# Performance work log

Hardware: AMD Instinct MI355X
Metric: run time of the kernel (lower is better)

The kernel has to match this reference:

```python
import jax, jax.numpy as jnp
import numpy as np

N = 10000   # nodes
E = 160000  # edges (before self-loops)
IN = 77     # input feature dim
H = 4       # heads (layers 1,2)
C = 128     # per-head out channels


def setup_inputs() -> dict:
    key = jax.random.key(0)
    ks = jax.random.split(key, 16)
    p = lambda k, shape: (jax.random.normal(k, shape, jnp.float32) * 0.1)
    z = lambda n: jnp.zeros((n,), jnp.float32)
    return {
        "x": jax.random.normal(ks[0], (N, IN), jnp.float32),
        "edge_index": jax.random.randint(ks[1], (2, E), 0, N),
        # layer 1: 77 -> H*C
        "Wl1": p(ks[2], (H * C, IN)), "bl1": z(H * C),
        "Wr1": p(ks[3], (H * C, IN)), "br1": z(H * C),
        "att1": p(ks[4], (H, C)), "b1": z(H * C),
        # layer 2: H*C -> H*C
        "Wl2": p(ks[5], (H * C, H * C)), "bl2": z(H * C),
        "Wr2": p(ks[6], (H * C, H * C)), "br2": z(H * C),
        "att2": p(ks[7], (H, C)), "b2": z(H * C),
        # layer 3: H*C -> C (1 head)
        "Wl3": p(ks[8], (C, H * C)), "bl3": z(C),
        "Wr3": p(ks[9], (C, H * C)), "br3": z(C),
        "att3": p(ks[10], (1, C)), "b3": z(C),
    }


def _gatv2_layer(x, src, dst, Wl, bl, Wr, br, att, bias, heads, outc):
    """PyG GATv2Conv (eval mode, self-loops already in src/dst, concat=True)."""
    n = x.shape[0]
    xl = (x @ Wl.T + bl).reshape(n, heads, outc)  # source transform
    xr = (x @ Wr.T + br).reshape(n, heads, outc)  # target transform
    # edge-wise score: a^T LeakyReLU(xl[src] + xr[dst])
    e = jax.nn.leaky_relu(xl[src] + xr[dst], negative_slope=0.2)  # [E,H,C]
    logits = jnp.einsum('ehc,hc->eh', e, att)                      # [E,H]
    # segment softmax over edges grouped by destination node
    m = jax.lax.stop_gradient(jax.ops.segment_max(logits, dst, num_segments=n))
    ev = jnp.exp(logits - m[dst])
    denom = jax.ops.segment_sum(ev, dst, num_segments=n)
    alpha = ev / (denom[dst] + 1e-16)                              # [E,H]
    # scatter-add weighted messages
    out = jax.ops.segment_sum(xl[src] * alpha[:, :, None], dst, num_segments=n)
    return out.reshape(n, heads * outc) + bias


def reference(x, edge_index, Wl1, bl1, Wr1, br1, att1, b1,
              Wl2, bl2, Wr2, br2, att2, b2,
              Wl3, bl3, Wr3, br3, att3, b3):
    n = x.shape[0]
    loop = jnp.arange(n)
    src = jnp.concatenate([edge_index[0], loop])  # add self-loops (PyG default)
    dst = jnp.concatenate([edge_index[1], loop])
    h = jax.nn.elu(_gatv2_layer(x, src, dst, Wl1, bl1, Wr1, br1, att1, b1, H, C))
    h = jax.nn.elu(_gatv2_layer(h, src, dst, Wl2, bl2, Wr2, br2, att2, b2, H, C))
    return _gatv2_layer(h, src, dst, Wl3, bl3, Wr3, br3, att3, b3, 1, C)
```

## Files before the change

### kernel.cpp

```cpp
#include <hip/hip_runtime.h>
#include <hip/hip_bf16.h>
#include <math.h>

typedef __attribute__((ext_vector_type(8))) short short8;
typedef __attribute__((ext_vector_type(4))) float f32x4;
typedef __attribute__((ext_vector_type(2))) float f32x2;
typedef __attribute__((ext_vector_type(4))) unsigned int u32x4;

__device__ __forceinline__ float bf2f(unsigned short u) {
  union { unsigned int i; float f; } x; x.i = ((unsigned int)u) << 16; return x.f;
}

__device__ __forceinline__ f32x2 pk_add(f32x2 a, f32x2 b) {
  f32x2 d; asm("v_pk_add_f32 %0, %1, %2" : "=v"(d) : "v"(a), "v"(b)); return d;
}
__device__ __forceinline__ f32x2 pk_mul(f32x2 a, f32x2 b) {
  f32x2 d; asm("v_pk_mul_f32 %0, %1, %2" : "=v"(d) : "v"(a), "v"(b)); return d;
}
__device__ __forceinline__ f32x2 pk_fma(f32x2 a, f32x2 b, f32x2 c) {
  f32x2 d; asm("v_pk_fma_f32 %0, %1, %2, %3" : "=v"(d) : "v"(a), "v"(b), "v"(c)); return d;
}
__device__ __forceinline__ f32x2 pk_abs(f32x2 a) {
  union { f32x2 f; unsigned int u[2]; } x; x.f = a;
  x.u[0] &= 0x7fffffffu; x.u[1] &= 0x7fffffffu;
  return x.f;
}
__device__ __forceinline__ f32x2 unpk(unsigned int w) {
  union { f32x2 f; unsigned int u[2]; } x;
  x.u[0] = w << 16;
  x.u[1] = w & 0xffff0000u;
  return x.f;
}

template <int CTRL>
__device__ __forceinline__ float dpp_add(float x) {
  int y = __builtin_amdgcn_update_dpp(0, __builtin_bit_cast(int, x), CTRL, 0xF, 0xF, true);
  return x + __builtin_bit_cast(float, y);
}
__device__ __forceinline__ float row16_sum(float p) {
  p = dpp_add<0xB1>(p);
  p = dpp_add<0x4E>(p);
  p = dpp_add<0x124>(p);
  p = dpp_add<0x128>(p);
  return p;
}

__device__ __forceinline__ void load_lds16(const void* g, void* l) {
  __builtin_amdgcn_global_load_lds(
      (const __attribute__((address_space(1))) unsigned int*)g,
      (__attribute__((address_space(3))) unsigned int*)l, 16, 0, 0);
}

__global__ __launch_bounds__(256) void gemm_mfma(
    const __hip_bfloat16* __restrict__ A, const __hip_bfloat16* __restrict__ B,
    const float* __restrict__ bl, const float* __restrict__ br, int halfN,
    __hip_bfloat16* __restrict__ out, int M, int K, int Nout) {
  __shared__ __hip_bfloat16 As[128 * 32];
  __shared__ __hip_bfloat16 Bs[128 * 32];
  int t = threadIdx.x;
  int w = t >> 6, l = t & 63;
  int lr = l & 15, lh = l >> 4;
  int wr = w >> 1, wc = w & 1;
  int m0 = blockIdx.y * 128, n0 = blockIdx.x * 128;
  f32x4 acc[4][4] = {};
  int nk = K >> 5;
  for (int ks = 0; ks < nk; ++ks) {
    int k0 = ks << 5;
#pragma unroll
    for (int p = 0; p < 2; ++p) {
      int c = p * 256 + t;
      int row = c >> 2, sub = c & 3;
      int gm = m0 + row; if (gm >= M) gm = M - 1;
      const __hip_bfloat16* gsrc = A + (size_t)gm * K + k0 + sub * 8;
      char* ldst = (char*)As + (size_t)(p * 256 + w * 64) * 16;
      load_lds16(gsrc, ldst);
    }
#pragma unroll
    for (int p = 0; p < 2; ++p) {
      int c = p * 256 + t;
      int row = c >> 2, sub = c & 3;
      const __hip_bfloat16* gsrc = B + (size_t)(n0 + row) * K + k0 + sub * 8;
      char* ldst = (char*)Bs + (size_t)(p * 256 + w * 64) * 16;
      load_lds16(gsrc, ldst);
    }
    __syncthreads();
    short8 af[4], bf[4];
#pragma unroll
    for (int mt = 0; mt < 4; ++mt)
      af[mt] = *(const short8*)(As + (size_t)(wr * 64 + mt * 16 + lr) * 32 + lh * 8);
#pragma unroll
    for (int nt = 0; nt < 4; ++nt)
      bf[nt] = *(const short8*)(Bs + (size_t)(wc * 64 + nt * 16 + lr) * 32 + lh * 8);
#pragma unroll
    for (int mt = 0; mt < 4; ++mt)
#pragma unroll
      for (int nt = 0; nt < 4; ++nt)
        acc[mt][nt] = __builtin_amdgcn_mfma_f32_16x16x32_bf16(af[mt], bf[nt], acc[mt][nt], 0, 0, 0);
    __syncthreads();
  }
#pragma unroll
  for (int mt = 0; mt < 4; ++mt) {
#pragma unroll
    for (int r = 0; r < 4; ++r) {
      int gm = m0 + wr * 64 + mt * 16 + lh * 4 + r;
      if (gm >= M) continue;
#pragma unroll
      for (int nt = 0; nt < 4; ++nt) {
        int gn = n0 + wc * 64 + nt * 16 + lr;
        float bv = (gn < halfN) ? bl[gn] : br[gn - halfN];
        out[(size_t)gm * Nout + gn] = __float2bfloat16(acc[mt][nt][r] + bv);
      }
    }
  }
}

struct CastSeg { const float* src; __hip_bfloat16* dst; int rows, K, Kp, row0, start; };
struct CastArgs { CastSeg s[7]; int total; };

__global__ __launch_bounds__(256) void k_cast_all(CastArgs A) {
  int stride = gridDim.x * blockDim.x;
  for (int i = blockIdx.x * blockDim.x + threadIdx.x; i < A.total; i += stride) {
    int si = 0;
#pragma unroll
    for (int j = 1; j < 7; j++) if (i >= A.s[j].start) si = j;
    CastSeg sg = A.s[si];
    int li = i - sg.start;
    int r = li / sg.Kp, k = li - r * sg.Kp;
    float v = (k < sg.K) ? sg.src[(size_t)r * sg.K + k] : 0.f;
    sg.dst[(size_t)(sg.row0 + r) * sg.Kp + k] = __float2bfloat16(v);
  }
}

__global__ void k_hist(const int* __restrict__ ei, int E, int N, int* __restrict__ deg) {
  int e = blockIdx.x * blockDim.x + threadIdx.x;
  int ET = E + N;
  if (e >= ET) return;
  int d = (e < E) ? ei[E + e] : (e - E);
  atomicAdd(&deg[d], 1);
}

__global__ __launch_bounds__(256) void k_scan_one(const int* __restrict__ deg, int N,
                                                  int* __restrict__ rp, int* __restrict__ cursor) {
  __shared__ int part[256];
  int t = threadIdx.x;
  int chunk = (N + 255) / 256;
  int lo = t * chunk;
  int hi = lo + chunk; if (hi > N) hi = N;
  int s = 0;
  for (int i = lo; i < hi; ++i) s += deg[i];
  part[t] = s;
  __syncthreads();
  for (int off = 1; off < 256; off <<= 1) {
    int x = (t >= off) ? part[t - off] : 0;
    __syncthreads();
    part[t] += x;
    __syncthreads();
  }
  int run = (t == 0) ? 0 : part[t - 1];
  for (int i = lo; i < hi; ++i) {
    rp[i] = run;
    cursor[i] = run;
    run += deg[i];
  }
  if (t == 255) rp[N] = run;
}

__global__ void k_scatter(const int* __restrict__ ei, int E, int N,
                          int* __restrict__ cursor, int* __restrict__ srcs) {
  int e = blockIdx.x * blockDim.x + threadIdx.x;
  int ET = E + N;
  if (e >= ET) return;
  int s = (e < E) ? ei[e] : (e - E);
  int d = (e < E) ? ei[E + e] : (e - E);
  int pos = atomicAdd(&cursor[d], 1);
  srcs[pos] = s;
}

template <int CPL> struct VecSel;
template <> struct VecSel<8> { using T = short8; };
template <> struct VecSel<2> { using T = unsigned int; };

template <int HC, int Hn, int LDc, bool ELU, typename OutT>
__global__ __launch_bounds__(256) void k_edge_fused(
    const __hip_bfloat16* __restrict__ xl, const __hip_bfloat16* __restrict__ xr,
    const int* __restrict__ rp, const int* __restrict__ srcs,
    const float* __restrict__ att, const float* __restrict__ bias,
    int N, OutT* __restrict__ out) {
  const int CPL = HC / 64;
  const int NP = CPL / 2;
  using VecT = typename VecSel<CPL>::T;
  int lane = threadIdx.x & 63;
  int n = (blockIdx.x * blockDim.x + threadIdx.x) >> 6;
  if (n >= N) return;

  f32x2 a06[NP], a04[NP], xrv2[NP];
#pragma unroll
  for (int p = 0; p < NP; ++p) {
    float alo = att[lane * CPL + 2 * p], ahi = att[lane * CPL + 2 * p + 1];
    a06[p].x = 0.6f * alo; a06[p].y = 0.6f * ahi;
    a04[p].x = 0.4f * alo; a04[p].y = 0.4f * ahi;
  }
  {
    const unsigned int* xw = (const unsigned int*)(xr + (size_t)n * LDc + lane * CPL);
#pragma unroll
    for (int p = 0; p < NP; ++p) xrv2[p] = unpk(xw[p]);
  }

  int s0 = rp[n], s1 = rp[n + 1];
  int len = s1 - s0;
  float m = -INFINITY, sum = 0.f;
  f32x2 acc2[NP];
#pragma unroll
  for (int p = 0; p < NP; ++p) { acc2[p].x = 0.f; acc2[p].y = 0.f; }

  auto loadrow = [&](int idx) -> VecT {
    return *(const VecT*)(xl + (size_t)srcs[s0 + idx] * LDc + lane * CPL);
  };
  auto proc = [&](VecT v) {
    unsigned int wv[NP];
    if constexpr (CPL == 8) {
      union { VecT s; u32x4 w; } u; u.s = v;
#pragma unroll
      for (int p = 0; p < NP; ++p) wv[p] = u.w[p];
    } else {
      wv[0] = (unsigned int)v;
    }
    f32x2 xv2[NP];
    f32x2 p2; p2.x = 0.f; p2.y = 0.f;
#pragma unroll
    for (int p = 0; p < NP; ++p) {
      xv2[p] = unpk(wv[p]);
      f32x2 s = pk_add(xv2[p], xrv2[p]);
      f32x2 sa = pk_abs(s);
      p2 = pk_fma(a06[p], s, p2);
      p2 = pk_fma(a04[p], sa, p2);
    }
    float pp = p2.x + p2.y;
    pp = row16_sum(pp);
    if constexpr (Hn == 1) {
      pp += __shfl_xor(pp, 16, 64);
      pp += __shfl_xor(pp, 32, 64);
    }
    if (__any(pp > m + 8.f)) {
      float mn = fmaxf(m, pp);
      float corr = __expf(m - mn);
      float wgt = __expf(pp - mn);
      sum = sum * corr + wgt;
      f32x2 corr2; corr2.x = corr; corr2.y = corr;
      f32x2 wgt2; wgt2.x = wgt; wgt2.y = wgt;
#pragma unroll
      for (int p = 0; p < NP; ++p)
        acc2[p] = pk_fma(acc2[p], corr2, pk_mul(wgt2, xv2[p]));
      m = mn;
    } else {
      float wgt = __expf(pp - m);
      sum += wgt;
      f32x2 wgt2; wgt2.x = wgt; wgt2.y = wgt;
#pragma unroll
      for (int p = 0; p < NP; ++p) acc2[p] = pk_fma(wgt2, xv2[p], acc2[p]);
    }
  };

  if (len > 0) {
    VecT b0, b1;
    b0 = loadrow(0);
    if (len > 1) b1 = loadrow(1);
    int i = 0;
    for (; i + 1 < len; i += 2) {
      VecT n0v, n1v;
      bool pf = (i + 2 < len);
      if (pf) {
        n0v = loadrow(i + 2);
        n1v = (i + 3 < len) ? loadrow(i + 3) : n0v;
      }
      proc(b0);
      proc(b1);
      if (pf) { b0 = n0v; b1 = n1v; }
    }
    if (i < len) proc(b0);
  }

  float inv = 1.f / (sum + 1e-16f);
#pragma unroll
  for (int p = 0; p < NP; ++p) {
    float r0 = acc2[p].x * inv + bias[lane * CPL + 2 * p];
    float r1 = acc2[p].y * inv + bias[lane * CPL + 2 * p + 1];
    if (ELU) {
      r0 = r0 > 0.f ? r0 : expm1f(r0);
      r1 = r1 > 0.f ? r1 : expm1f(r1);
    }
    acc2[p].x = r0; acc2[p].y = r1;
  }
  if constexpr (sizeof(OutT) == 2) {
    short8 o;
#pragma unroll
    for (int p = 0; p < NP; ++p) {
      __hip_bfloat16 b0 = __float2bfloat16(acc2[p].x);
      __hip_bfloat16 b1 = __float2bfloat16(acc2[p].y);
      o[2 * p] = __builtin_bit_cast(short, b0);
      o[2 * p + 1] = __builtin_bit_cast(short, b1);
    }
    *(short8*)((__hip_bfloat16*)out + (size_t)n * HC + lane * CPL) = o;
  } else {
    f32x2 o; o.x = acc2[0].x; o.y = acc2[0].y;
    *(f32x2*)((float*)out + (size_t)n * HC + lane * 2) = o;
  }
}

extern "C" void kernel_launch(void* const* d_in, const int* in_sizes, int n_in,
                              void* d_out, int out_size, void* d_ws, size_t ws_size,
                              hipStream_t stream) {
  const int IN = 77, Kp1 = 96, Hh = 4, Cc = 128, HC = Hh * Cc;
  const int N = in_sizes[0] / IN;
  const int E = in_sizes[1] / 2;
  const int ET = E + N;

  const float* x   = (const float*)d_in[0];
  const int*   ei  = (const int*)d_in[1];
  const float* Wl1 = (const float*)d_in[2];  const float* bl1 = (const float*)d_in[3];
  const float* Wr1 = (const float*)d_in[4];  const float* br1 = (const float*)d_in[5];
  const float* att1= (const float*)d_in[6];  const float* b1  = (const float*)d_in[7];
  const float* Wl2 = (const float*)d_in[8];  const float* bl2 = (const float*)d_in[9];
  const float* Wr2 = (const float*)d_in[10]; const float* br2 = (const float*)d_in[11];
  const float* att2= (const float*)d_in[12]; const float* b2  = (const float*)d_in[13];
  const float* Wl3 = (const float*)d_in[14]; const float* bl3 = (const float*)d_in[15];
  const float* Wr3 = (const float*)d_in[16]; const float* br3 = (const float*)d_in[17];
  const float* att3= (const float*)d_in[18]; const float* b3  = (const float*)d_in[19];
  float* out = (float*)d_out;

  char* w = (char*)d_ws;
  size_t off = 0;
  auto alloc = [&](size_t bytes) -> void* {
    void* p = w + off;
    off += (bytes + 255) & ~(size_t)255;
    return p;
  };
  __hip_bfloat16* xlr = (__hip_bfloat16*)alloc((size_t)N * 2 * HC * 2);
  __hip_bfloat16* hb  = (__hip_bfloat16*)alloc((size_t)N * HC * 2);
  __hip_bfloat16* Wc1 = (__hip_bfloat16*)alloc((size_t)2 * HC * Kp1 * 2);
  __hip_bfloat16* Wc2 = (__hip_bfloat16*)alloc((size_t)2 * HC * HC * 2);
  __hip_bfloat16* Wc3 = (__hip_bfloat16*)alloc((size_t)2 * Cc * HC * 2);
  int*   deg    = (int*)alloc((size_t)N * 4);
  int*   rp     = (int*)alloc((size_t)(N + 1) * 4);
  int*   cursor = (int*)alloc((size_t)N * 4);
  int*   srcs   = (int*)alloc((size_t)ET * 4);

  CastArgs CA;
  int cum = 0;
  auto seg = [&](int idx, const float* src, __hip_bfloat16* dst, int rows, int K, int Kp, int row0) {
    CA.s[idx] = {src, dst, rows, K, Kp, row0, cum};
    cum += rows * Kp;
  };
  seg(0, Wl1, Wc1, HC, IN, Kp1, 0);
  seg(1, Wr1, Wc1, HC, IN, Kp1, HC);
  seg(2, Wl2, Wc2, HC, HC, HC, 0);
  seg(3, Wr2, Wc2, HC, HC, HC, HC);
  seg(4, Wl3, Wc3, Cc, HC, HC, 0);
  seg(5, Wr3, Wc3, Cc, HC, HC, Cc);
  seg(6, x,   hb,  N,  IN, Kp1, 0);
  CA.total = cum;
  k_cast_all<<<1024, 256, 0, stream>>>(CA);

  hipMemsetAsync(deg, 0, (size_t)N * 4, stream);
  int tb = 256;
  k_hist<<<(ET + tb - 1) / tb, tb, 0, stream>>>(ei, E, N, deg);
  k_scan_one<<<1, 256, 0, stream>>>(deg, N, rp, cursor);
  k_scatter<<<(ET + tb - 1) / tb, tb, 0, stream>>>(ei, E, N, cursor, srcs);

  int nodeBlocks = (N + 3) / 4;
  int mb = (N + 127) / 128;

  {
    dim3 g(2 * HC / 128, mb);
    gemm_mfma<<<g, 256, 0, stream>>>(hb, Wc1, bl1, br1, HC, xlr, N, Kp1, 2 * HC);
    k_edge_fused<512, 4, 1024, true, __hip_bfloat16><<<nodeBlocks, 256, 0, stream>>>(
        xlr, xlr + HC, rp, srcs, att1, b1, N, hb);
  }
  {
    dim3 g(2 * HC / 128, mb);
    gemm_mfma<<<g, 256, 0, stream>>>(hb, Wc2, bl2, br2, HC, xlr, N, HC, 2 * HC);
    k_edge_fused<512, 4, 1024, true, __hip_bfloat16><<<nodeBlocks, 256, 0, stream>>>(
        xlr, xlr + HC, rp, srcs, att2, b2, N, hb);
  }
  {
    dim3 g(2 * Cc / 128, mb);
    gemm_mfma<<<g, 256, 0, stream>>>(hb, Wc3, bl3, br3, Cc, xlr, N, HC, 2 * Cc);
    k_edge_fused<128, 1, 256, false, float><<<nodeBlocks, 256, 0, stream>>>(
        xlr, xlr + Cc, rp, srcs, att3, b3, N, out);
  }
}
```

Measured before the change: 221.9 us.

## Process nodes in degree-sorted order and fuse cast with degree histogram

Adds a bucket sort of nodes by in-degree, largest first, inside the single-block scan kernel. Each edge-aggregation wavefront now takes its node through this permutation, so the four wavefronts in a block see similar degrees and long-degree nodes start early. The weight/input cast and the degree histogram are merged into one grid-stride kernel to save a launch. The cost is extra serial work in the one-block scan, an indirection load per wave, and output writes and xr reads that are no longer in node order.

```diff
diff --git a/kernel.cpp b/kernel.cpp
--- a/kernel.cpp
+++ b/kernel.cpp
@@ -117,9 +117,11 @@
 struct CastSeg { const float* src; __hip_bfloat16* dst; int rows, K, Kp, row0, start; };
 struct CastArgs { CastSeg s[7]; int total; };
 
-__global__ __launch_bounds__(256) void k_cast_all(CastArgs A) {
+__global__ __launch_bounds__(256) void k_prep(CastArgs A, const int* __restrict__ ei,
+                                              int E, int N, int* __restrict__ deg) {
   int stride = gridDim.x * blockDim.x;
-  for (int i = blockIdx.x * blockDim.x + threadIdx.x; i < A.total; i += stride) {
+  int tid0 = blockIdx.x * blockDim.x + threadIdx.x;
+  for (int i = tid0; i < A.total; i += stride) {
     int si = 0;
 #pragma unroll
     for (int j = 1; j < 7; j++) if (i >= A.s[j].start) si = j;
@@ -129,19 +131,19 @@
     float v = (k < sg.K) ? sg.src[(size_t)r * sg.K + k] : 0.f;
     sg.dst[(size_t)(sg.row0 + r) * sg.Kp + k] = __float2bfloat16(v);
   }
-}
-
-__global__ void k_hist(const int* __restrict__ ei, int E, int N, int* __restrict__ deg) {
-  int e = blockIdx.x * blockDim.x + threadIdx.x;
   int ET = E + N;
-  if (e >= ET) return;
-  int d = (e < E) ? ei[E + e] : (e - E);
-  atomicAdd(&deg[d], 1);
-}
-
-__global__ __launch_bounds__(256) void k_scan_one(const int* __restrict__ deg, int N,
-                                                  int* __restrict__ rp, int* __restrict__ cursor) {
+  for (int e = tid0; e < ET; e += stride) {
+    int d = (e < E) ? ei[E + e] : (e - E);
+    atomicAdd(&deg[d], 1);
+  }
+}
+
+__global__ __launch_bounds__(256) void k_scan_perm(const int* __restrict__ deg, int N,
+                                                   int* __restrict__ rp, int* __restrict__ cursor,
+                                                   int* __restrict__ perm) {
   __shared__ int part[256];
+  __shared__ int bcnt[64];
+  __shared__ int boff[64];
   int t = threadIdx.x;
   int chunk = (N + 255) / 256;
   int lo = t * chunk;
@@ -149,6 +151,7 @@
   int s = 0;
   for (int i = lo; i < hi; ++i) s += deg[i];
   part[t] = s;
+  if (t < 64) bcnt[t] = 0;
   __syncthreads();
   for (int off = 1; off < 256; off <<= 1) {
     int x = (t >= off) ? part[t - off] : 0;
@@ -161,8 +164,21 @@
     rp[i] = run;
     cursor[i] = run;
     run += deg[i];
+    int b = deg[i] < 63 ? deg[i] : 63;
+    atomicAdd(&bcnt[b], 1);
   }
   if (t == 255) rp[N] = run;
+  __syncthreads();
+  if (t == 0) {
+    int acc = 0;
+    for (int b = 63; b >= 0; --b) { boff[b] = acc; acc += bcnt[b]; }
+  }
+  __syncthreads();
+  for (int i = lo; i < hi; ++i) {
+    int b = deg[i] < 63 ? deg[i] : 63;
+    int pos = atomicAdd(&boff[b], 1);
+    perm[pos] = i;
+  }
 }
 
 __global__ void k_scatter(const int* __restrict__ ei, int E, int N,
@@ -184,14 +200,16 @@
 __global__ __launch_bounds__(256) void k_edge_fused(
     const __hip_bfloat16* __restrict__ xl, const __hip_bfloat16* __restrict__ xr,
     const int* __restrict__ rp, const int* __restrict__ srcs,
+    const int* __restrict__ perm,
     const float* __restrict__ att, const float* __restrict__ bias,
     int N, OutT* __restrict__ out) {
   const int CPL = HC / 64;
   const int NP = CPL / 2;
   using VecT = typename VecSel<CPL>::T;
   int lane = threadIdx.x & 63;
-  int n = (blockIdx.x * blockDim.x + threadIdx.x) >> 6;
-  if (n >= N) return;
+  int nw = (blockIdx.x * blockDim.x + threadIdx.x) >> 6;
+  if (nw >= N) return;
+  int n = perm[nw];
 
   f32x2 a06[NP], a04[NP], xrv2[NP];
 #pragma unroll
@@ -344,6 +362,7 @@
   int*   rp     = (int*)alloc((size_t)(N + 1) * 4);
   int*   cursor = (int*)alloc((size_t)N * 4);
   int*   srcs   = (int*)alloc((size_t)ET * 4);
+  int*   perm   = (int*)alloc((size_t)N * 4);
 
   CastArgs CA;
   int cum = 0;
@@ -359,13 +378,11 @@
   seg(5, Wr3, Wc3, Cc, HC, HC, Cc);
   seg(6, x,   hb,  N,  IN, Kp1, 0);
   CA.total = cum;
-  k_cast_all<<<1024, 256, 0, stream>>>(CA);
 
   hipMemsetAsync(deg, 0, (size_t)N * 4, stream);
-  int tb = 256;
-  k_hist<<<(ET + tb - 1) / tb, tb, 0, stream>>>(ei, E, N, deg);
-  k_scan_one<<<1, 256, 0, stream>>>(deg, N, rp, cursor);
-  k_scatter<<<(ET + tb - 1) / tb, tb, 0, stream>>>(ei, E, N, cursor, srcs);
+  k_prep<<<1024, 256, 0, stream>>>(CA, ei, E, N, deg);
+  k_scan_perm<<<1, 256, 0, stream>>>(deg, N, rp, cursor, perm);
+  k_scatter<<<(ET + 255) / 256, 256, 0, stream>>>(ei, E, N, cursor, srcs);
 
   int nodeBlocks = (N + 3) / 4;
   int mb = (N + 127) / 128;
@@ -374,18 +391,18 @@
     dim3 g(2 * HC / 128, mb);
     gemm_mfma<<<g, 256, 0, stream>>>(hb, Wc1, bl1, br1, HC, xlr, N, Kp1, 2 * HC);
     k_edge_fused<512, 4, 1024, true, __hip_bfloat16><<<nodeBlocks, 256, 0, stream>>>(
-        xlr, xlr + HC, rp, srcs, att1, b1, N, hb);
+        xlr, xlr + HC, rp, srcs, perm, att1, b1, N, hb);
   }
   {
     dim3 g(2 * HC / 128, mb);
     gemm_mfma<<<g, 256, 0, stream>>>(hb, Wc2, bl2, br2, HC, xlr, N, HC, 2 * HC);
     k_edge_fused<512, 4, 1024, true, __hip_bfloat16><<<nodeBlocks, 256, 0, stream>>>(
-        xlr, xlr + HC, rp, srcs, att2, b2, N, hb);
+        xlr, xlr + HC, rp, srcs, perm, att2, b2, N, hb);
   }
   {
     dim3 g(2 * Cc / 128, mb);
     gemm_mfma<<<g, 256, 0, stream>>>(hb, Wc3, bl3, br3, Cc, xlr, N, HC, 2 * Cc);
     k_edge_fused<128, 1, 256, false, float><<<nodeBlocks, 256, 0, stream>>>(
-        xlr, xlr + Cc, rp, srcs, att3, b3, N, out);
-  }
-}
+        xlr, xlr + Cc, rp, srcs, perm, att3, b3, N, out);
+  }
+}
```

Result: faster. 214.0 us (-3.5%).
